# Optimization experiments

Hardware: AMD Instinct MI355X
Metric: run time of the kernel (lower is better)

The kernel has to match this reference:

```python
import jax, jax.numpy as jnp
import numpy as np

D_MODEL, Q, V, H = 1024, 64, 64, 16
B, K = 2, 2048


def setup_inputs() -> dict:
    key = jax.random.key(0)
    ks = jax.random.split(key, 8)
    s = 0.02
    return {
        "xi": jax.random.normal(ks[0], (B, K, D_MODEL), dtype=jnp.float32),
        # stacked per-head projection weights (equivalent to h separate nn.Linear)
        "Wq": jax.random.normal(ks[1], (H, D_MODEL, Q), dtype=jnp.float32) * s,
        "bq": jax.random.normal(ks[2], (H, Q), dtype=jnp.float32) * s,
        "Wk": jax.random.normal(ks[3], (H, D_MODEL, Q), dtype=jnp.float32) * s,
        "bk": jax.random.normal(ks[4], (H, Q), dtype=jnp.float32) * s,
        "Wv": jax.random.normal(ks[5], (H, D_MODEL, V), dtype=jnp.float32) * s,
        "bv": jax.random.normal(ks[6], (H, V), dtype=jnp.float32) * s,
        "Wo": jax.random.normal(ks[7], (H * V, D_MODEL), dtype=jnp.float32) * s,
        "bo": jnp.zeros((D_MODEL,), dtype=jnp.float32),
    }


def reference(xi, Wq, bq, Wk, bk, Wv, bv, Wo, bo):
    # per-head projections, batched over heads: [B,H,K,q]
    queries = jnp.einsum("bkd,hdq->bhkq", xi, Wq) + bq[None, :, None, :]
    keys = jnp.einsum("bkd,hdq->bhkq", xi, Wk) + bk[None, :, None, :]
    values = jnp.einsum("bkd,hdv->bhkv", xi, Wv) + bv[None, :, None, :]
    # NOTE: original scales by sqrt(queries.shape[1]) == sqrt(seq_len K), not sqrt(q)
    scale = 1.0 / np.sqrt(xi.shape[1]).astype(np.float32)
    scores = jax.nn.softmax(jnp.einsum("bhkq,bhmq->bhkm", queries, keys) * scale, axis=-1)
    attn = jnp.einsum("bhkm,bhmv->bhkv", scores, values)  # [B,H,K,v]
    # concat heads along last dim -> [B,K,H*v]
    attn = attn.transpose(0, 2, 1, 3).reshape(xi.shape[0], xi.shape[1], -1)
    return attn @ Wo + bo
```

## Files before the change

### kernel.cpp

```cpp
#include <hip/hip_runtime.h>
#include <math.h>

typedef __bf16 bf16x8 __attribute__((ext_vector_type(8)));
typedef float  f32x4  __attribute__((ext_vector_type(4)));
typedef float  f32x16 __attribute__((ext_vector_type(16)));
typedef unsigned short u16x8 __attribute__((ext_vector_type(8)));

#define D_MODEL 1024
#define QDIM    64
#define HEADS   16
#define BATCH   2
#define SEQ     2048
#define M_ROWS  (BATCH*SEQ)
#define NCAT    (HEADS*3*QDIM)

__device__ __forceinline__ unsigned short f2bf(float f) {
    unsigned int u = __float_as_uint(f);
    u += 0x7fffu + ((u >> 16) & 1u);
    return (unsigned short)(u >> 16);
}

__device__ __forceinline__ void gl16(const unsigned short* g, unsigned short* l) {
    __builtin_amdgcn_global_load_lds(
        (const __attribute__((address_space(1))) unsigned int*)g,
        (__attribute__((address_space(3))) unsigned int*)l, 16, 0, 0);
}

__global__ __launch_bounds__(256) void k_cvt_bf16(const float* __restrict__ in,
                                                  unsigned short* __restrict__ out) {
    int i = (blockIdx.x * 256 + threadIdx.x) * 8;
    f32x4 a = *(const f32x4*)(in + i);
    f32x4 b = *(const f32x4*)(in + i + 4);
    u16x8 o;
    o[0]=f2bf(a[0]); o[1]=f2bf(a[1]); o[2]=f2bf(a[2]); o[3]=f2bf(a[3]);
    o[4]=f2bf(b[0]); o[5]=f2bf(b[1]); o[6]=f2bf(b[2]); o[7]=f2bf(b[3]);
    *(u16x8*)(out + i) = o;
}

__global__ __launch_bounds__(256) void k_prep_w(const float* __restrict__ Wq,
                                                const float* __restrict__ Wk,
                                                const float* __restrict__ Wv,
                                                const float* __restrict__ bq,
                                                const float* __restrict__ bk,
                                                const float* __restrict__ bv,
                                                const float* __restrict__ Wo,
                                                unsigned short* __restrict__ WcatT,
                                                float* __restrict__ bcat,
                                                unsigned short* __restrict__ WoT,
                                                float qscale) {
    __shared__ float t[64][65];
    int tid = threadIdx.x;
    int dr = tid >> 2, qc = (tid & 3) * 16;
    if (blockIdx.x < 768) {
        int blk = blockIdx.x;
        int dt = blk & 15, h = (blk >> 4) & 15, s = blk >> 8;
        const float* W = (s == 0) ? Wq : (s == 1) ? Wk : Wv;
        float sc = (s == 0) ? qscale : 1.0f;
        const float* src = W + (size_t)h * (D_MODEL * QDIM) + (size_t)(dt * 64 + dr) * QDIM + qc;
#pragma unroll
        for (int j = 0; j < 4; ++j) {
            f32x4 v = *(const f32x4*)(src + j * 4);
            t[dr][qc + j * 4 + 0] = v[0]; t[dr][qc + j * 4 + 1] = v[1];
            t[dr][qc + j * 4 + 2] = v[2]; t[dr][qc + j * 4 + 3] = v[3];
        }
        __syncthreads();
        int q = tid >> 2, dc = (tid & 3) * 16;
        unsigned short* dst = WcatT + (size_t)(h * 192 + s * 64 + q) * D_MODEL + dt * 64 + dc;
#pragma unroll
        for (int j = 0; j < 2; ++j) {
            u16x8 o;
#pragma unroll
            for (int e = 0; e < 8; ++e) o[e] = f2bf(t[dc + j * 8 + e][q] * sc);
            *(u16x8*)(dst + j * 8) = o;
        }
        if (dt == 0 && tid < 64) {
            const float* bb = (s == 0) ? bq : (s == 1) ? bk : bv;
            bcat[h * 192 + s * 64 + tid] = bb[h * QDIM + tid] * sc;
        }
    } else {
        int blk = blockIdx.x - 768;
        int ct = blk & 15, rt = blk >> 4;
        const float* src = Wo + (size_t)(rt * 64 + dr) * D_MODEL + ct * 64 + qc;
#pragma unroll
        for (int j = 0; j < 4; ++j) {
            f32x4 v = *(const f32x4*)(src + j * 4);
            t[dr][qc + j * 4 + 0] = v[0]; t[dr][qc + j * 4 + 1] = v[1];
            t[dr][qc + j * 4 + 2] = v[2]; t[dr][qc + j * 4 + 3] = v[3];
        }
        __syncthreads();
        int q = tid >> 2, dc = (tid & 3) * 16;
        unsigned short* dst = WoT + (size_t)(ct * 64 + q) * D_MODEL + rt * 64 + dc;
#pragma unroll
        for (int j = 0; j < 2; ++j) {
            u16x8 o;
#pragma unroll
            for (int e = 0; e < 8; ++e) o[e] = f2bf(t[dc + j * 8 + e][q]);
            *(u16x8*)(dst + j * 8) = o;
        }
    }
}

template<bool OUT_BF16>
__global__ __launch_bounds__(256) void k_gemm(const unsigned short* __restrict__ A,
                                              const unsigned short* __restrict__ BT,
                                              const float* __restrict__ bias,
                                              void* __restrict__ Cout,
                                              int N, int Kd) {
    __shared__ __align__(16) unsigned char smem[65536];
    const int tid = threadIdx.x;
    const int lane = tid & 63, w = tid >> 6;
    const int g = lane >> 4, c = lane & 15;
    int nwg = gridDim.x * gridDim.y;
    int bid = blockIdx.y * gridDim.x + blockIdx.x;
    int sw = (bid & 7) * (nwg >> 3) + (bid >> 3);
    int bx = sw % gridDim.x, by = sw / gridDim.x;
    const int m0 = by * 128, n0 = bx * 128;
    const int wm = (w >> 1) * 64, wn = (w & 1) * 64;
    f32x4 acc[4][4] = {};

    const int srow = w * 16 + (lane >> 2);
    const int scol = ((lane & 3) ^ ((lane >> 3) & 3)) * 8;
    const unsigned short* pA0 = A  + (size_t)(m0 + srow) * Kd + scol;
    const unsigned short* pA1 = pA0 + (size_t)64 * Kd;
    const unsigned short* pB0 = BT + (size_t)(n0 + srow) * Kd + scol;
    const unsigned short* pB1 = pB0 + (size_t)64 * Kd;
    const int kc = (c >> 1) & 3;
    const int aoff = (wm + c) * 64 + ((g ^ kc) * 16);
    const int boff = (wn + c) * 64 + ((g ^ kc) * 16);

#define STAGE(buf)                                                                   \
    {                                                                                \
        unsigned short* lb = (unsigned short*)(smem + (buf) * 16384) + w * 512;      \
        gl16(pA0, lb);                                                               \
        gl16(pA1, lb + 2048);                                                        \
        gl16(pB0, lb + 4096);                                                        \
        gl16(pB1, lb + 6144);                                                        \
        pA0 += 32; pA1 += 32; pB0 += 32; pB1 += 32;                                  \
    }

#define COMPUTE(buf)                                                                 \
    {                                                                                \
        const unsigned char* Ab = smem + (buf) * 16384;                              \
        const unsigned char* Bb = Ab + 8192;                                         \
        bf16x8 af[4], bfr[4];                                                        \
        _Pragma("unroll") for (int mf = 0; mf < 4; ++mf)                             \
            af[mf] = *(const bf16x8*)(Ab + mf * 1024 + aoff);                        \
        _Pragma("unroll") for (int nf = 0; nf < 4; ++nf)                             \
            bfr[nf] = *(const bf16x8*)(Bb + nf * 1024 + boff);                       \
        __builtin_amdgcn_s_setprio(1);                                               \
        _Pragma("unroll") for (int mf = 0; mf < 4; ++mf)                             \
            _Pragma("unroll") for (int nf = 0; nf < 4; ++nf)                         \
                acc[mf][nf] = __builtin_amdgcn_mfma_f32_16x16x32_bf16(               \
                    af[mf], bfr[nf], acc[mf][nf], 0, 0, 0);                          \
        __builtin_amdgcn_s_setprio(0);                                               \
    }

    const int nt = Kd >> 5;
    STAGE(0); STAGE(1); STAGE(2);

    for (int t = 0; t < nt - 3; ++t) {
        STAGE((t + 3) & 3);
        asm volatile("s_waitcnt vmcnt(12)" ::: "memory");
        __builtin_amdgcn_s_barrier();
        __builtin_amdgcn_sched_barrier(0);
        COMPUTE(t & 3);
        __builtin_amdgcn_sched_barrier(0);
        __builtin_amdgcn_s_barrier();
    }
    asm volatile("s_waitcnt vmcnt(8)" ::: "memory");
    __builtin_amdgcn_s_barrier();
    __builtin_amdgcn_sched_barrier(0);
    COMPUTE((nt - 3) & 3);
    __builtin_amdgcn_sched_barrier(0);
    __builtin_amdgcn_s_barrier();
    asm volatile("s_waitcnt vmcnt(4)" ::: "memory");
    __builtin_amdgcn_s_barrier();
    __builtin_amdgcn_sched_barrier(0);
    COMPUTE((nt - 2) & 3);
    __builtin_amdgcn_sched_barrier(0);
    __builtin_amdgcn_s_barrier();
    asm volatile("s_waitcnt vmcnt(0)" ::: "memory");
    __builtin_amdgcn_s_barrier();
    __builtin_amdgcn_sched_barrier(0);
    COMPUTE((nt - 1) & 3);
#undef STAGE
#undef COMPUTE

#pragma unroll
    for (int mf = 0; mf < 4; ++mf)
#pragma unroll
        for (int nf = 0; nf < 4; ++nf) {
            int col = n0 + wn + nf * 16 + c;
            float bb = bias[col];
#pragma unroll
            for (int r = 0; r < 4; ++r) {
                int row = m0 + wm + mf * 16 + 4 * g + r;
                float v = acc[mf][nf][r] + bb;
                if (OUT_BF16)
                    ((unsigned short*)Cout)[(size_t)row * N + col] = f2bf(v);
                else
                    ((float*)Cout)[(size_t)row * N + col] = v;
            }
        }
}

__global__ __launch_bounds__(256) void k_repack(const unsigned short* __restrict__ qkv,
                                                unsigned short* __restrict__ kfrag,
                                                unsigned short* __restrict__ vfrag) {
    int blk = blockIdx.x;
    int kt = blk & 31, h = (blk >> 5) & 15, b = blk >> 9;
    __shared__ unsigned short ktile[64][72];
    __shared__ unsigned short vtile[64][72];
    int tid = threadIdx.x;
#pragma unroll
    for (int j = 0; j < 2; ++j) {
        int cid = tid + j * 256;
        int row = cid >> 3, ch = (cid & 7) * 8;
        const unsigned short* base = qkv + (size_t)(b * SEQ + kt * 64 + row) * NCAT + h * 192;
        *(u16x8*)&ktile[row][ch] = *(const u16x8*)(base + 64 + ch);
        *(u16x8*)&vtile[row][ch] = *(const u16x8*)(base + 128 + ch);
    }
    __syncthreads();
    size_t obase = (size_t)blk * 4096;
#pragma unroll
    for (int j = 0; j < 2; ++j) {
        int p = tid + j * 256;
        int f = p >> 6, l31 = p & 31, hi = (p >> 5) & 1;
        *(u16x8*)(kfrag + obase + p * 8) =
            *(const u16x8*)&ktile[(f >> 2) * 32 + l31][(f & 3) * 16 + hi * 8];
        int vv = (f & 1) * 32 + l31;
        int k0 = (f >> 2) * 32 + ((f >> 1) & 1) * 16 + hi * 8;
        u16x8 o;
#pragma unroll
        for (int e = 0; e < 8; ++e) o[e] = vtile[k0 + e][vv];
        *(u16x8*)(vfrag + obase + p * 8) = o;
    }
}

__global__ __launch_bounds__(256) void k_attn(const unsigned short* __restrict__ qkv,
                                              const unsigned short* __restrict__ kfrag,
                                              const unsigned short* __restrict__ vfrag,
                                              unsigned short* __restrict__ attn) {
    int bid = blockIdx.x;
    int blk = (bid & 7) * 128 + (bid >> 3);
    int qt = blk & 31, h = (blk >> 5) & 15, b = blk >> 9;
    int tid = threadIdx.x, w = tid >> 6, lane = tid & 63;
    int l31 = lane & 31, hi = lane >> 5;
    int qh = w & 1, kh = w >> 1;

    __shared__ float red[4096];
    __shared__ float rsb[128];

    const int qbase = b * SEQ + qt * 64;
    const unsigned short* qrow = qkv + (size_t)(qbase + qh * 32 + l31) * NCAT + h * 192;
    bf16x8 qf0 = *(const bf16x8*)(qrow + 0 * 16 + hi * 8);
    bf16x8 qf1 = *(const bf16x8*)(qrow + 1 * 16 + hi * 8);
    bf16x8 qf2 = *(const bf16x8*)(qrow + 2 * 16 + hi * 8);
    bf16x8 qf3 = *(const bf16x8*)(qrow + 3 * 16 + hi * 8);

    f32x16 o0 = {}, o1 = {};
    float rsum = 0.f;

    const size_t fb = (size_t)(b * 512 + h * 32) * 4096 + (size_t)(kh * 4) * 512 + lane * 8;
    const unsigned short* kp = kfrag + fb;
    const unsigned short* vp = vfrag + fb;

    bf16x8 aK0, aK1, aK2, aK3, aV0, aV1, aV2, aV3;
    bf16x8 bK0, bK1, bK2, bK3, bV0, bV1, bV2, bV3;

#define LOADT(K0, K1, K2, K3, V0, V1, V2, V3)                   \
    {                                                           \
        K0 = *(const bf16x8*)(kp);                              \
        K1 = *(const bf16x8*)(kp + 512);                        \
        K2 = *(const bf16x8*)(kp + 1024);                       \
        K3 = *(const bf16x8*)(kp + 1536);                       \
        V0 = *(const bf16x8*)(vp);                              \
        V1 = *(const bf16x8*)(vp + 512);                        \
        V2 = *(const bf16x8*)(vp + 1024);                       \
        V3 = *(const bf16x8*)(vp + 1536);                       \
        kp += 4096; vp += 4096;                                 \
    }

#define COMPUTE(K0, K1, K2, K3, V0, V1, V2, V3)                                       \
    {                                                                                 \
        f32x16 st = {};                                                               \
        st = __builtin_amdgcn_mfma_f32_32x32x16_bf16(K0, qf0, st, 0, 0, 0);           \
        st = __builtin_amdgcn_mfma_f32_32x32x16_bf16(K1, qf1, st, 0, 0, 0);           \
        st = __builtin_amdgcn_mfma_f32_32x32x16_bf16(K2, qf2, st, 0, 0, 0);           \
        st = __builtin_amdgcn_mfma_f32_32x32x16_bf16(K3, qf3, st, 0, 0, 0);           \
        _Pragma("unroll") for (int r = 0; r < 16; ++r) {                              \
            float p = __builtin_amdgcn_exp2f(st[r]);                                  \
            st[r] = p;                                                                \
            rsum += p;                                                                \
        }                                                                             \
        unsigned int d0, d1, d2, d3, d4, d5, d6, d7;                                  \
        asm("v_cvt_pk_bf16_f32 %0, %1, %2" : "=v"(d0) : "v"(st[0]),  "v"(st[1]));     \
        asm("v_cvt_pk_bf16_f32 %0, %1, %2" : "=v"(d1) : "v"(st[2]),  "v"(st[3]));     \
        asm("v_cvt_pk_bf16_f32 %0, %1, %2" : "=v"(d2) : "v"(st[4]),  "v"(st[5]));     \
        asm("v_cvt_pk_bf16_f32 %0, %1, %2" : "=v"(d3) : "v"(st[6]),  "v"(st[7]));     \
        asm("v_cvt_pk_bf16_f32 %0, %1, %2" : "=v"(d4) : "v"(st[8]),  "v"(st[9]));     \
        asm("v_cvt_pk_bf16_f32 %0, %1, %2" : "=v"(d5) : "v"(st[10]), "v"(st[11]));    \
        asm("v_cvt_pk_bf16_f32 %0, %1, %2" : "=v"(d6) : "v"(st[12]), "v"(st[13]));    \
        asm("v_cvt_pk_bf16_f32 %0, %1, %2" : "=v"(d7) : "v"(st[14]), "v"(st[15]));    \
        asm("v_permlane32_swap_b32 %0, %1" : "+v"(d0), "+v"(d2));                     \
        asm("v_permlane32_swap_b32 %0, %1" : "+v"(d1), "+v"(d3));                     \
        asm("v_permlane32_swap_b32 %0, %1" : "+v"(d4), "+v"(d6));                     \
        asm("v_permlane32_swap_b32 %0, %1" : "+v"(d5), "+v"(d7));                     \
        union { unsigned int u[4]; bf16x8 v; } pa0, pa1;                              \
        pa0.u[0] = d0; pa0.u[1] = d1; pa0.u[2] = d2; pa0.u[3] = d3;                   \
        pa1.u[0] = d4; pa1.u[1] = d5; pa1.u[2] = d6; pa1.u[3] = d7;                   \
        o0 = __builtin_amdgcn_mfma_f32_32x32x16_bf16(pa0.v, V0, o0, 0, 0, 0);         \
        o1 = __builtin_amdgcn_mfma_f32_32x32x16_bf16(pa0.v, V1, o1, 0, 0, 0);         \
        o0 = __builtin_amdgcn_mfma_f32_32x32x16_bf16(pa1.v, V2, o0, 0, 0, 0);         \
        o1 = __builtin_amdgcn_mfma_f32_32x32x16_bf16(pa1.v, V3, o1, 0, 0, 0);         \
    }

    LOADT(aK0, aK1, aK2, aK3, aV0, aV1, aV2, aV3);

    const int NT = SEQ / 64;
    for (int t = 0; t < NT; t += 2) {
        LOADT(bK0, bK1, bK2, bK3, bV0, bV1, bV2, bV3);
        COMPUTE(aK0, aK1, aK2, aK3, aV0, aV1, aV2, aV3);
        if (t + 2 < NT)
            LOADT(aK0, aK1, aK2, aK3, aV0, aV1, aV2, aV3);
        COMPUTE(bK0, bK1, bK2, bK3, bV0, bV1, bV2, bV3);
    }
#undef LOADT
#undef COMPUTE

    rsum += __shfl_xor(rsum, 32);
    if (kh == 1) {
#pragma unroll
        for (int r = 0; r < 16; ++r) {
            int q = (r & 3) + 8 * (r >> 2) + 4 * hi;
            red[(qh * 32 + q) * 64 + l31]      = o0[r];
            red[(qh * 32 + q) * 64 + 32 + l31] = o1[r];
        }
    }
    if (lane < 32) rsb[(kh * 2 + qh) * 32 + l31] = rsum;
    __syncthreads();
    if (kh == 0) {
#pragma unroll
        for (int r = 0; r < 16; ++r) {
            int q = (r & 3) + 8 * (r >> 2) + 4 * hi;
            float tot = rsb[qh * 32 + q] + rsb[(2 + qh) * 32 + q];
            float inv = 1.0f / tot;
            float v0 = (o0[r] + red[(qh * 32 + q) * 64 + l31]) * inv;
            float v1 = (o1[r] + red[(qh * 32 + q) * 64 + 32 + l31]) * inv;
            int row = qbase + qh * 32 + q;
            attn[(size_t)row * (HEADS * QDIM) + h * QDIM + l31]      = f2bf(v0);
            attn[(size_t)row * (HEADS * QDIM) + h * QDIM + 32 + l31] = f2bf(v1);
        }
    }
}

extern "C" void kernel_launch(void* const* d_in, const int* in_sizes, int n_in,
                              void* d_out, int out_size, void* d_ws, size_t ws_size,
                              hipStream_t stream) {
    const float* xi = (const float*)d_in[0];
    const float* Wq = (const float*)d_in[1];
    const float* bq = (const float*)d_in[2];
    const float* Wk = (const float*)d_in[3];
    const float* bk = (const float*)d_in[4];
    const float* Wv = (const float*)d_in[5];
    const float* bv = (const float*)d_in[6];
    const float* Wo = (const float*)d_in[7];
    const float* bo = (const float*)d_in[8];

    unsigned short* xi_bf = (unsigned short*)d_ws;
    unsigned short* WcatT = xi_bf + (size_t)M_ROWS * D_MODEL;
    unsigned short* WoT   = WcatT + (size_t)NCAT * D_MODEL;
    float*          bcat  = (float*)(WoT + (size_t)D_MODEL * D_MODEL);
    unsigned short* qkvc  = (unsigned short*)(bcat + NCAT);
    unsigned short* kfrag = qkvc + (size_t)M_ROWS * NCAT;
    unsigned short* vfrag = kfrag + (size_t)BATCH * HEADS * 32 * 4096;
    unsigned short* attnb = vfrag + (size_t)BATCH * HEADS * 32 * 4096;

    float qscale = 1.4426950408889634f / sqrtf((float)SEQ);

    k_cvt_bf16<<<(M_ROWS * D_MODEL) / 2048, 256, 0, stream>>>(xi, xi_bf);
    k_prep_w<<<1024, 256, 0, stream>>>(Wq, Wk, Wv, bq, bk, bv, Wo, WcatT, bcat, WoT, qscale);

    k_gemm<true><<<dim3(NCAT / 128, M_ROWS / 128), 256, 0, stream>>>(
        xi_bf, WcatT, bcat, (void*)qkvc, NCAT, D_MODEL);

    k_repack<<<BATCH * HEADS * (SEQ / 64), 256, 0, stream>>>(qkvc, kfrag, vfrag);

    k_attn<<<BATCH * HEADS * (SEQ / 64), 256, 0, stream>>>(qkvc, kfrag, vfrag, attnb);

    k_gemm<false><<<dim3(D_MODEL / 128, M_ROWS / 128), 256, 0, stream>>>(
        attnb, WoT, bo, d_out, D_MODEL, D_MODEL);
}
```

Baseline: 119.6 us.

## Software-pipeline attention loop so QK^T MFMA of next tile overlaps exp/PV

Splits the per-tile attention body into separate QK^T, exp/pack and PV stages and interleaves them across two key tiles. The QK^T MFMAs of the second tile are issued before the PV MFMAs of the first, so matrix-core work overlaps the exp and conversion VALU work. V fragments now use one shared register set loaded just before use instead of double-buffered, which lowers register pressure but exposes V load latency more. Adds a second score accumulator, which raises live registers.

```diff
diff --git a/kernel.cpp b/kernel.cpp
--- a/kernel.cpp
+++ b/kernel.cpp
@@ -265,68 +265,87 @@
     const unsigned short* kp = kfrag + fb;
     const unsigned short* vp = vfrag + fb;
 
-    bf16x8 aK0, aK1, aK2, aK3, aV0, aV1, aV2, aV3;
-    bf16x8 bK0, bK1, bK2, bK3, bV0, bV1, bV2, bV3;
-
-#define LOADT(K0, K1, K2, K3, V0, V1, V2, V3)                   \
+    bf16x8 aK0, aK1, aK2, aK3, bK0, bK1, bK2, bK3;
+    bf16x8 v0, v1, v2, v3;
+    f32x16 sa, sb;
+    union PU { unsigned int u[4]; bf16x8 v; } paa0, paa1, pab0, pab1;
+
+#define LOADK(K0, K1, K2, K3)                                   \
     {                                                           \
         K0 = *(const bf16x8*)(kp);                              \
         K1 = *(const bf16x8*)(kp + 512);                        \
         K2 = *(const bf16x8*)(kp + 1024);                       \
         K3 = *(const bf16x8*)(kp + 1536);                       \
-        V0 = *(const bf16x8*)(vp);                              \
-        V1 = *(const bf16x8*)(vp + 512);                        \
-        V2 = *(const bf16x8*)(vp + 1024);                       \
-        V3 = *(const bf16x8*)(vp + 1536);                       \
-        kp += 4096; vp += 4096;                                 \
-    }
-
-#define COMPUTE(K0, K1, K2, K3, V0, V1, V2, V3)                                       \
+        kp += 4096;                                             \
+    }
+#define LOADV()                                                 \
+    {                                                           \
+        v0 = *(const bf16x8*)(vp);                              \
+        v1 = *(const bf16x8*)(vp + 512);                        \
+        v2 = *(const bf16x8*)(vp + 1024);                       \
+        v3 = *(const bf16x8*)(vp + 1536);                       \
+        vp += 4096;                                             \
+    }
+#define QKT(S, K0, K1, K2, K3)                                              \
+    {                                                                       \
+        S = (f32x16){};                                                     \
+        S = __builtin_amdgcn_mfma_f32_32x32x16_bf16(K0, qf0, S, 0, 0, 0);   \
+        S = __builtin_amdgcn_mfma_f32_32x32x16_bf16(K1, qf1, S, 0, 0, 0);   \
+        S = __builtin_amdgcn_mfma_f32_32x32x16_bf16(K2, qf2, S, 0, 0, 0);   \
+        S = __builtin_amdgcn_mfma_f32_32x32x16_bf16(K3, qf3, S, 0, 0, 0);   \
+    }
+#define EXPPACK(S, PA0, PA1)                                                          \
     {                                                                                 \
-        f32x16 st = {};                                                               \
-        st = __builtin_amdgcn_mfma_f32_32x32x16_bf16(K0, qf0, st, 0, 0, 0);           \
-        st = __builtin_amdgcn_mfma_f32_32x32x16_bf16(K1, qf1, st, 0, 0, 0);           \
-        st = __builtin_amdgcn_mfma_f32_32x32x16_bf16(K2, qf2, st, 0, 0, 0);           \
-        st = __builtin_amdgcn_mfma_f32_32x32x16_bf16(K3, qf3, st, 0, 0, 0);           \
         _Pragma("unroll") for (int r = 0; r < 16; ++r) {                              \
-            float p = __builtin_amdgcn_exp2f(st[r]);                                  \
-            st[r] = p;                                                                \
+            float p = __builtin_amdgcn_exp2f(S[r]);                                   \
+            S[r] = p;                                                                 \
             rsum += p;                                                                \
         }                                                                             \
         unsigned int d0, d1, d2, d3, d4, d5, d6, d7;                                  \
-        asm("v_cvt_pk_bf16_f32 %0, %1, %2" : "=v"(d0) : "v"(st[0]),  "v"(st[1]));     \
-        asm("v_cvt_pk_bf16_f32 %0, %1, %2" : "=v"(d1) : "v"(st[2]),  "v"(st[3]));     \
-        asm("v_cvt_pk_bf16_f32 %0, %1, %2" : "=v"(d2) : "v"(st[4]),  "v"(st[5]));     \
-        asm("v_cvt_pk_bf16_f32 %0, %1, %2" : "=v"(d3) : "v"(st[6]),  "v"(st[7]));     \
-        asm("v_cvt_pk_bf16_f32 %0, %1, %2" : "=v"(d4) : "v"(st[8]),  "v"(st[9]));     \
-        asm("v_cvt_pk_bf16_f32 %0, %1, %2" : "=v"(d5) : "v"(st[10]), "v"(st[11]));    \
-        asm("v_cvt_pk_bf16_f32 %0, %1, %2" : "=v"(d6) : "v"(st[12]), "v"(st[13]));    \
-        asm("v_cvt_pk_bf16_f32 %0, %1, %2" : "=v"(d7) : "v"(st[14]), "v"(st[15]));    \
+        asm("v_cvt_pk_bf16_f32 %0, %1, %2" : "=v"(d0) : "v"(S[0]),  "v"(S[1]));       \
+        asm("v_cvt_pk_bf16_f32 %0, %1, %2" : "=v"(d1) : "v"(S[2]),  "v"(S[3]));       \
+        asm("v_cvt_pk_bf16_f32 %0, %1, %2" : "=v"(d2) : "v"(S[4]),  "v"(S[5]));       \
+        asm("v_cvt_pk_bf16_f32 %0, %1, %2" : "=v"(d3) : "v"(S[6]),  "v"(S[7]));       \
+        asm("v_cvt_pk_bf16_f32 %0, %1, %2" : "=v"(d4) : "v"(S[8]),  "v"(S[9]));       \
+        asm("v_cvt_pk_bf16_f32 %0, %1, %2" : "=v"(d5) : "v"(S[10]), "v"(S[11]));      \
+        asm("v_cvt_pk_bf16_f32 %0, %1, %2" : "=v"(d6) : "v"(S[12]), "v"(S[13]));      \
+        asm("v_cvt_pk_bf16_f32 %0, %1, %2" : "=v"(d7) : "v"(S[14]), "v"(S[15]));      \
         asm("v_permlane32_swap_b32 %0, %1" : "+v"(d0), "+v"(d2));                     \
         asm("v_permlane32_swap_b32 %0, %1" : "+v"(d1), "+v"(d3));                     \
         asm("v_permlane32_swap_b32 %0, %1" : "+v"(d4), "+v"(d6));                     \
         asm("v_permlane32_swap_b32 %0, %1" : "+v"(d5), "+v"(d7));                     \
-        union { unsigned int u[4]; bf16x8 v; } pa0, pa1;                              \
-        pa0.u[0] = d0; pa0.u[1] = d1; pa0.u[2] = d2; pa0.u[3] = d3;                   \
-        pa1.u[0] = d4; pa1.u[1] = d5; pa1.u[2] = d6; pa1.u[3] = d7;                   \
-        o0 = __builtin_amdgcn_mfma_f32_32x32x16_bf16(pa0.v, V0, o0, 0, 0, 0);         \
-        o1 = __builtin_amdgcn_mfma_f32_32x32x16_bf16(pa0.v, V1, o1, 0, 0, 0);         \
-        o0 = __builtin_amdgcn_mfma_f32_32x32x16_bf16(pa1.v, V2, o0, 0, 0, 0);         \
-        o1 = __builtin_amdgcn_mfma_f32_32x32x16_bf16(pa1.v, V3, o1, 0, 0, 0);         \
-    }
-
-    LOADT(aK0, aK1, aK2, aK3, aV0, aV1, aV2, aV3);
+        PA0.u[0] = d0; PA0.u[1] = d1; PA0.u[2] = d2; PA0.u[3] = d3;                   \
+        PA1.u[0] = d4; PA1.u[1] = d5; PA1.u[2] = d6; PA1.u[3] = d7;                   \
+    }
+#define PV(PA0, PA1)                                                                  \
+    {                                                                                 \
+        o0 = __builtin_amdgcn_mfma_f32_32x32x16_bf16(PA0.v, v0, o0, 0, 0, 0);         \
+        o1 = __builtin_amdgcn_mfma_f32_32x32x16_bf16(PA0.v, v1, o1, 0, 0, 0);         \
+        o0 = __builtin_amdgcn_mfma_f32_32x32x16_bf16(PA1.v, v2, o0, 0, 0, 0);         \
+        o1 = __builtin_amdgcn_mfma_f32_32x32x16_bf16(PA1.v, v3, o1, 0, 0, 0);         \
+    }
+
+    LOADK(aK0, aK1, aK2, aK3);
 
     const int NT = SEQ / 64;
     for (int t = 0; t < NT; t += 2) {
-        LOADT(bK0, bK1, bK2, bK3, bV0, bV1, bV2, bV3);
-        COMPUTE(aK0, aK1, aK2, aK3, aV0, aV1, aV2, aV3);
+        LOADV();
+        LOADK(bK0, bK1, bK2, bK3);
+        QKT(sa, aK0, aK1, aK2, aK3);
+        EXPPACK(sa, paa0, paa1);
         if (t + 2 < NT)
-            LOADT(aK0, aK1, aK2, aK3, aV0, aV1, aV2, aV3);
-        COMPUTE(bK0, bK1, bK2, bK3, bV0, bV1, bV2, bV3);
-    }
-#undef LOADT
-#undef COMPUTE
+            LOADK(aK0, aK1, aK2, aK3);
+        QKT(sb, bK0, bK1, bK2, bK3);
+        PV(paa0, paa1);
+        LOADV();
+        EXPPACK(sb, pab0, pab1);
+        PV(pab0, pab1);
+    }
+#undef LOADK
+#undef LOADV
+#undef QKT
+#undef EXPPACK
+#undef PV
 
     rsum += __shfl_xor(rsum, 32);
     if (kh == 1) {
@@ -345,11 +364,11 @@
             int q = (r & 3) + 8 * (r >> 2) + 4 * hi;
             float tot = rsb[qh * 32 + q] + rsb[(2 + qh) * 32 + q];
             float inv = 1.0f / tot;
-            float v0 = (o0[r] + red[(qh * 32 + q) * 64 + l31]) * inv;
-            float v1 = (o1[r] + red[(qh * 32 + q) * 64 + 32 + l31]) * inv;
+            float v0e = (o0[r] + red[(qh * 32 + q) * 64 + l31]) * inv;
+            float v1e = (o1[r] + red[(qh * 32 + q) * 64 + 32 + l31]) * inv;
             int row = qbase + qh * 32 + q;
-            attn[(size_t)row * (HEADS * QDIM) + h * QDIM + l31]      = f2bf(v0);
-            attn[(size_t)row * (HEADS * QDIM) + h * QDIM + 32 + l31] = f2bf(v1);
+            attn[(size_t)row * (HEADS * QDIM) + h * QDIM + l31]      = f2bf(v0e);
+            attn[(size_t)row * (HEADS * QDIM) + h * QDIM + 32 + l31] = f2bf(v1e);
         }
     }
 }
```

Result: no change. 120.2 us (+0.6%).

## Merge input conversion into weight prep and restructure GEMM to double-buffered BK=64

Applied to the files above, without the earlier changes.

Folds the xi fp32-to-bf16 conversion into the weight-prep kernel as extra blocks, which removes one kernel launch. The GEMM K-loop changes from a 4-stage, BK=32 pipeline to a 2-stage, BK=64 double buffer with an XOR-swizzled LDS layout and two MFMA sub-steps per tile. LDS use stays at 64KB. The shallower pipeline may hide less global-load latency, though each barrier now covers more compute.

```diff
diff --git a/kernel.cpp b/kernel.cpp
--- a/kernel.cpp
+++ b/kernel.cpp
@@ -26,33 +26,34 @@
         (__attribute__((address_space(3))) unsigned int*)l, 16, 0, 0);
 }
 
-__global__ __launch_bounds__(256) void k_cvt_bf16(const float* __restrict__ in,
-                                                  unsigned short* __restrict__ out) {
-    int i = (blockIdx.x * 256 + threadIdx.x) * 8;
-    f32x4 a = *(const f32x4*)(in + i);
-    f32x4 b = *(const f32x4*)(in + i + 4);
-    u16x8 o;
-    o[0]=f2bf(a[0]); o[1]=f2bf(a[1]); o[2]=f2bf(a[2]); o[3]=f2bf(a[3]);
-    o[4]=f2bf(b[0]); o[5]=f2bf(b[1]); o[6]=f2bf(b[2]); o[7]=f2bf(b[3]);
-    *(u16x8*)(out + i) = o;
-}
-
-__global__ __launch_bounds__(256) void k_prep_w(const float* __restrict__ Wq,
+__global__ __launch_bounds__(256) void k_prep_w(const float* __restrict__ xi,
+                                                const float* __restrict__ Wq,
                                                 const float* __restrict__ Wk,
                                                 const float* __restrict__ Wv,
                                                 const float* __restrict__ bq,
                                                 const float* __restrict__ bk,
                                                 const float* __restrict__ bv,
                                                 const float* __restrict__ Wo,
+                                                unsigned short* __restrict__ xi_bf,
                                                 unsigned short* __restrict__ WcatT,
                                                 float* __restrict__ bcat,
                                                 unsigned short* __restrict__ WoT,
                                                 float qscale) {
+    int tid = threadIdx.x;
+    if (blockIdx.x < 2048) {
+        int i = (blockIdx.x * 256 + tid) * 8;
+        f32x4 a = *(const f32x4*)(xi + i);
+        f32x4 b = *(const f32x4*)(xi + i + 4);
+        u16x8 o;
+        o[0]=f2bf(a[0]); o[1]=f2bf(a[1]); o[2]=f2bf(a[2]); o[3]=f2bf(a[3]);
+        o[4]=f2bf(b[0]); o[5]=f2bf(b[1]); o[6]=f2bf(b[2]); o[7]=f2bf(b[3]);
+        *(u16x8*)(xi_bf + i) = o;
+        return;
+    }
     __shared__ float t[64][65];
-    int tid = threadIdx.x;
     int dr = tid >> 2, qc = (tid & 3) * 16;
-    if (blockIdx.x < 768) {
-        int blk = blockIdx.x;
+    if (blockIdx.x < 2816) {
+        int blk = blockIdx.x - 2048;
         int dt = blk & 15, h = (blk >> 4) & 15, s = blk >> 8;
         const float* W = (s == 0) ? Wq : (s == 1) ? Wk : Wv;
         float sc = (s == 0) ? qscale : 1.0f;
@@ -78,7 +79,7 @@
             bcat[h * 192 + s * 64 + tid] = bb[h * QDIM + tid] * sc;
         }
     } else {
-        int blk = blockIdx.x - 768;
+        int blk = blockIdx.x - 2816;
         int ct = blk & 15, rt = blk >> 4;
         const float* src = Wo + (size_t)(rt * 64 + dr) * D_MODEL + ct * 64 + qc;
 #pragma unroll
@@ -106,7 +107,8 @@
                                               const float* __restrict__ bias,
                                               void* __restrict__ Cout,
                                               int N, int Kd) {
-    __shared__ __align__(16) unsigned char smem[65536];
+    __shared__ __align__(16) unsigned short Alds[2][128 * 64];
+    __shared__ __align__(16) unsigned short Blds[2][128 * 64];
     const int tid = threadIdx.x;
     const int lane = tid & 63, w = tid >> 6;
     const int g = lane >> 4, c = lane & 15;
@@ -116,73 +118,58 @@
     int bx = sw % gridDim.x, by = sw / gridDim.x;
     const int m0 = by * 128, n0 = bx * 128;
     const int wm = (w >> 1) * 64, wn = (w & 1) * 64;
+    const int r8 = lane >> 3, chx = (lane & 7) ^ r8;
+    const int swz = c & 7;
     f32x4 acc[4][4] = {};
 
-    const int srow = w * 16 + (lane >> 2);
-    const int scol = ((lane & 3) ^ ((lane >> 3) & 3)) * 8;
-    const unsigned short* pA0 = A  + (size_t)(m0 + srow) * Kd + scol;
-    const unsigned short* pA1 = pA0 + (size_t)64 * Kd;
-    const unsigned short* pB0 = BT + (size_t)(n0 + srow) * Kd + scol;
-    const unsigned short* pB1 = pB0 + (size_t)64 * Kd;
-    const int kc = (c >> 1) & 3;
-    const int aoff = (wm + c) * 64 + ((g ^ kc) * 16);
-    const int boff = (wn + c) * 64 + ((g ^ kc) * 16);
-
-#define STAGE(buf)                                                                   \
-    {                                                                                \
-        unsigned short* lb = (unsigned short*)(smem + (buf) * 16384) + w * 512;      \
-        gl16(pA0, lb);                                                               \
-        gl16(pA1, lb + 2048);                                                        \
-        gl16(pB0, lb + 4096);                                                        \
-        gl16(pB1, lb + 6144);                                                        \
-        pA0 += 32; pA1 += 32; pB0 += 32; pB1 += 32;                                  \
-    }
-
-#define COMPUTE(buf)                                                                 \
-    {                                                                                \
-        const unsigned char* Ab = smem + (buf) * 16384;                              \
-        const unsigned char* Bb = Ab + 8192;                                         \
-        bf16x8 af[4], bfr[4];                                                        \
-        _Pragma("unroll") for (int mf = 0; mf < 4; ++mf)                             \
-            af[mf] = *(const bf16x8*)(Ab + mf * 1024 + aoff);                        \
-        _Pragma("unroll") for (int nf = 0; nf < 4; ++nf)                             \
-            bfr[nf] = *(const bf16x8*)(Bb + nf * 1024 + boff);                       \
-        __builtin_amdgcn_s_setprio(1);                                               \
-        _Pragma("unroll") for (int mf = 0; mf < 4; ++mf)                             \
-            _Pragma("unroll") for (int nf = 0; nf < 4; ++nf)                         \
-                acc[mf][nf] = __builtin_amdgcn_mfma_f32_16x16x32_bf16(               \
-                    af[mf], bfr[nf], acc[mf][nf], 0, 0, 0);                          \
-        __builtin_amdgcn_s_setprio(0);                                               \
-    }
-
-    const int nt = Kd >> 5;
-    STAGE(0); STAGE(1); STAGE(2);
-
-    for (int t = 0; t < nt - 3; ++t) {
-        STAGE((t + 3) & 3);
-        asm volatile("s_waitcnt vmcnt(12)" ::: "memory");
+    const unsigned short* pA = A  + (size_t)m0 * Kd;
+    const unsigned short* pB = BT + (size_t)n0 * Kd;
+    int k0 = 0;
+
+#define STAGE(buf)                                                                       \
+    {                                                                                    \
+        _Pragma("unroll") for (int i = 0; i < 4; ++i) {                                  \
+            int row = w * 32 + i * 8 + r8;                                               \
+            gl16(pA + (size_t)row * Kd + k0 + chx * 8, &Alds[buf][w * 2048 + i * 512]);  \
+            gl16(pB + (size_t)row * Kd + k0 + chx * 8, &Blds[buf][w * 2048 + i * 512]);  \
+        }                                                                                \
+        k0 += 64;                                                                        \
+    }
+
+#define COMPUTE(buf)                                                                     \
+    {                                                                                    \
+        _Pragma("unroll") for (int kk = 0; kk < 2; ++kk) {                               \
+            bf16x8 af[4], bfr[4];                                                        \
+            _Pragma("unroll") for (int mf = 0; mf < 4; ++mf)                             \
+                af[mf] = *(const bf16x8*)(&Alds[buf][(wm + mf * 16 + c) * 64 +           \
+                                                     (((kk * 4 + g) ^ swz) * 8)]);      \
+            _Pragma("unroll") for (int nf = 0; nf < 4; ++nf)                             \
+                bfr[nf] = *(const bf16x8*)(&Blds[buf][(wn + nf * 16 + c) * 64 +          \
+                                                      (((kk * 4 + g) ^ swz) * 8)]);     \
+            __builtin_amdgcn_s_setprio(1);                                               \
+            _Pragma("unroll") for (int mf = 0; mf < 4; ++mf)                             \
+                _Pragma("unroll") for (int nf = 0; nf < 4; ++nf)                         \
+                    acc[mf][nf] = __builtin_amdgcn_mfma_f32_16x16x32_bf16(               \
+                        af[mf], bfr[nf], acc[mf][nf], 0, 0, 0);                          \
+            __builtin_amdgcn_s_setprio(0);                                               \
+        }                                                                                \
+    }
+
+    const int nt = Kd >> 6;
+    STAGE(0);
+    for (int t = 0; t < nt; ++t) {
+        if (t + 1 < nt) {
+            STAGE((t + 1) & 1);
+            asm volatile("s_waitcnt vmcnt(8)" ::: "memory");
+        } else {
+            asm volatile("s_waitcnt vmcnt(0)" ::: "memory");
+        }
         __builtin_amdgcn_s_barrier();
         __builtin_amdgcn_sched_barrier(0);
-        COMPUTE(t & 3);
+        COMPUTE(t & 1);
         __builtin_amdgcn_sched_barrier(0);
         __builtin_amdgcn_s_barrier();
     }
-    asm volatile("s_waitcnt vmcnt(8)" ::: "memory");
-    __builtin_amdgcn_s_barrier();
-    __builtin_amdgcn_sched_barrier(0);
-    COMPUTE((nt - 3) & 3);
-    __builtin_amdgcn_sched_barrier(0);
-    __builtin_amdgcn_s_barrier();
-    asm volatile("s_waitcnt vmcnt(4)" ::: "memory");
-    __builtin_amdgcn_s_barrier();
-    __builtin_amdgcn_sched_barrier(0);
-    COMPUTE((nt - 2) & 3);
-    __builtin_amdgcn_sched_barrier(0);
-    __builtin_amdgcn_s_barrier();
-    asm volatile("s_waitcnt vmcnt(0)" ::: "memory");
-    __builtin_amdgcn_s_barrier();
-    __builtin_amdgcn_sched_barrier(0);
-    COMPUTE((nt - 1) & 3);
 #undef STAGE
 #undef COMPUTE
 
@@ -345,11 +332,11 @@
             int q = (r & 3) + 8 * (r >> 2) + 4 * hi;
             float tot = rsb[qh * 32 + q] + rsb[(2 + qh) * 32 + q];
             float inv = 1.0f / tot;
-            float v0 = (o0[r] + red[(qh * 32 + q) * 64 + l31]) * inv;
-            float v1 = (o1[r] + red[(qh * 32 + q) * 64 + 32 + l31]) * inv;
+            float v0e = (o0[r] + red[(qh * 32 + q) * 64 + l31]) * inv;
+            float v1e = (o1[r] + red[(qh * 32 + q) * 64 + 32 + l31]) * inv;
             int row = qbase + qh * 32 + q;
-            attn[(size_t)row * (HEADS * QDIM) + h * QDIM + l31]      = f2bf(v0);
-            attn[(size_t)row * (HEADS * QDIM) + h * QDIM + 32 + l31] = f2bf(v1);
+            attn[(size_t)row * (HEADS * QDIM) + h * QDIM + l31]      = f2bf(v0e);
+            attn[(size_t)row * (HEADS * QDIM) + h * QDIM + 32 + l31] = f2bf(v1e);
         }
     }
 }
@@ -378,8 +365,8 @@
 
     float qscale = 1.4426950408889634f / sqrtf((float)SEQ);
 
-    k_cvt_bf16<<<(M_ROWS * D_MODEL) / 2048, 256, 0, stream>>>(xi, xi_bf);
-    k_prep_w<<<1024, 256, 0, stream>>>(Wq, Wk, Wv, bq, bk, bv, Wo, WcatT, bcat, WoT, qscale);
+    k_prep_w<<<3072, 256, 0, stream>>>(xi, Wq, Wk, Wv, bq, bk, bv, Wo,
+                                       xi_bf, WcatT, bcat, WoT, qscale);
 
     k_gemm<true><<<dim3(NCAT / 128, M_ROWS / 128), 256, 0, stream>>>(
         xi_bf, WcatT, bcat, (void*)qkvc, NCAT, D_MODEL);
```

New measurement: 127.8 us. 1.07x slower.

## Fuse K/V fragment repack into QKV projection GEMM epilogue

Applied to the files above, without the earlier changes.

The QKV GEMM epilogue now writes K and V values straight into the MFMA fragment layouts used by the attention kernel, and only Q goes to the concatenated qkv buffer. This removes the separate repack kernel launch and its read-back of K/V from global memory. In exchange, the epilogue does scattered 2-byte and 8-byte stores with per-element index arithmetic, which may coalesce worse than the previous row-major writes.

```diff
diff --git a/kernel.cpp b/kernel.cpp
--- a/kernel.cpp
+++ b/kernel.cpp
@@ -5,6 +5,7 @@
 typedef float  f32x4  __attribute__((ext_vector_type(4)));
 typedef float  f32x16 __attribute__((ext_vector_type(16)));
 typedef unsigned short u16x8 __attribute__((ext_vector_type(8)));
+typedef unsigned short u16x4 __attribute__((ext_vector_type(4)));
 
 #define D_MODEL 1024
 #define QDIM    64
@@ -100,11 +101,13 @@
     }
 }
 
-template<bool OUT_BF16>
+template<bool FUSED>
 __global__ __launch_bounds__(256) void k_gemm(const unsigned short* __restrict__ A,
                                               const unsigned short* __restrict__ BT,
                                               const float* __restrict__ bias,
                                               void* __restrict__ Cout,
+                                              unsigned short* __restrict__ kfrag,
+                                              unsigned short* __restrict__ vfrag,
                                               int N, int Kd) {
     __shared__ __align__(16) unsigned char smem[65536];
     const int tid = threadIdx.x;
@@ -187,53 +190,50 @@
 #undef COMPUTE
 
 #pragma unroll
-    for (int mf = 0; mf < 4; ++mf)
+    for (int mf = 0; mf < 4; ++mf) {
+        const int row0 = m0 + wm + mf * 16 + 4 * g;
+        const int bb_  = row0 >> 11;
+        const int s_   = row0 & 2047;
+        const int tile = s_ >> 6;
+        const int krb  = s_ & 63;
 #pragma unroll
         for (int nf = 0; nf < 4; ++nf) {
             int col = n0 + wn + nf * 16 + c;
-            float bb = bias[col];
-#pragma unroll
-            for (int r = 0; r < 4; ++r) {
-                int row = m0 + wm + mf * 16 + 4 * g + r;
-                float v = acc[mf][nf][r] + bb;
-                if (OUT_BF16)
-                    ((unsigned short*)Cout)[(size_t)row * N + col] = f2bf(v);
-                else
-                    ((float*)Cout)[(size_t)row * N + col] = v;
+            float bv = bias[col];
+            if (!FUSED) {
+#pragma unroll
+                for (int r = 0; r < 4; ++r)
+                    ((float*)Cout)[(size_t)(row0 + r) * N + col] = acc[mf][nf][r] + bv;
+            } else {
+                unsigned short q0 = f2bf(acc[mf][nf][0] + bv);
+                unsigned short q1 = f2bf(acc[mf][nf][1] + bv);
+                unsigned short q2 = f2bf(acc[mf][nf][2] + bv);
+                unsigned short q3 = f2bf(acc[mf][nf][3] + bv);
+                int h   = col / 192;
+                int rem = col - h * 192;
+                int kind = rem >> 6;
+                int d   = rem & 63;
+                if (kind == 0) {
+                    unsigned short* p = (unsigned short*)Cout + (size_t)row0 * NCAT + col;
+                    p[0] = q0; p[NCAT] = q1; p[2 * NCAT] = q2; p[3 * NCAT] = q3;
+                } else {
+                    size_t obase = (size_t)(bb_ * 512 + h * 32 + tile) * 4096;
+                    if (kind == 1) {
+                        int f  = (krb >> 5) * 4 + (d >> 4);
+                        int hi = (d >> 3) & 1;
+                        unsigned short* p = kfrag + obase + f * 512 + hi * 256 +
+                                            (size_t)(krb & 31) * 8 + (d & 7);
+                        p[0] = q0; p[8] = q1; p[16] = q2; p[24] = q3;
+                    } else {
+                        int f  = (krb >> 5) * 4 + ((krb >> 4) & 1) * 2 + (d >> 5);
+                        int hi = (krb >> 3) & 1;
+                        u16x4 pk = {q0, q1, q2, q3};
+                        *(u16x4*)(vfrag + obase + f * 512 + hi * 256 +
+                                  (size_t)(d & 31) * 8 + (krb & 7)) = pk;
+                    }
+                }
             }
         }
-}
-
-__global__ __launch_bounds__(256) void k_repack(const unsigned short* __restrict__ qkv,
-                                                unsigned short* __restrict__ kfrag,
-                                                unsigned short* __restrict__ vfrag) {
-    int blk = blockIdx.x;
-    int kt = blk & 31, h = (blk >> 5) & 15, b = blk >> 9;
-    __shared__ unsigned short ktile[64][72];
-    __shared__ unsigned short vtile[64][72];
-    int tid = threadIdx.x;
-#pragma unroll
-    for (int j = 0; j < 2; ++j) {
-        int cid = tid + j * 256;
-        int row = cid >> 3, ch = (cid & 7) * 8;
-        const unsigned short* base = qkv + (size_t)(b * SEQ + kt * 64 + row) * NCAT + h * 192;
-        *(u16x8*)&ktile[row][ch] = *(const u16x8*)(base + 64 + ch);
-        *(u16x8*)&vtile[row][ch] = *(const u16x8*)(base + 128 + ch);
-    }
-    __syncthreads();
-    size_t obase = (size_t)blk * 4096;
-#pragma unroll
-    for (int j = 0; j < 2; ++j) {
-        int p = tid + j * 256;
-        int f = p >> 6, l31 = p & 31, hi = (p >> 5) & 1;
-        *(u16x8*)(kfrag + obase + p * 8) =
-            *(const u16x8*)&ktile[(f >> 2) * 32 + l31][(f & 3) * 16 + hi * 8];
-        int vv = (f & 1) * 32 + l31;
-        int k0 = (f >> 2) * 32 + ((f >> 1) & 1) * 16 + hi * 8;
-        u16x8 o;
-#pragma unroll
-        for (int e = 0; e < 8; ++e) o[e] = vtile[k0 + e][vv];
-        *(u16x8*)(vfrag + obase + p * 8) = o;
     }
 }
 
@@ -345,11 +345,11 @@
             int q = (r & 3) + 8 * (r >> 2) + 4 * hi;
             float tot = rsb[qh * 32 + q] + rsb[(2 + qh) * 32 + q];
             float inv = 1.0f / tot;
-            float v0 = (o0[r] + red[(qh * 32 + q) * 64 + l31]) * inv;
-            float v1 = (o1[r] + red[(qh * 32 + q) * 64 + 32 + l31]) * inv;
+            float v0e = (o0[r] + red[(qh * 32 + q) * 64 + l31]) * inv;
+            float v1e = (o1[r] + red[(qh * 32 + q) * 64 + 32 + l31]) * inv;
             int row = qbase + qh * 32 + q;
-            attn[(size_t)row * (HEADS * QDIM) + h * QDIM + l31]      = f2bf(v0);
-            attn[(size_t)row * (HEADS * QDIM) + h * QDIM + 32 + l31] = f2bf(v1);
+            attn[(size_t)row * (HEADS * QDIM) + h * QDIM + l31]      = f2bf(v0e);
+            attn[(size_t)row * (HEADS * QDIM) + h * QDIM + 32 + l31] = f2bf(v1e);
         }
     }
 }
@@ -382,12 +382,10 @@
     k_prep_w<<<1024, 256, 0, stream>>>(Wq, Wk, Wv, bq, bk, bv, Wo, WcatT, bcat, WoT, qscale);
 
     k_gemm<true><<<dim3(NCAT / 128, M_ROWS / 128), 256, 0, stream>>>(
-        xi_bf, WcatT, bcat, (void*)qkvc, NCAT, D_MODEL);
-
-    k_repack<<<BATCH * HEADS * (SEQ / 64), 256, 0, stream>>>(qkvc, kfrag, vfrag);
+        xi_bf, WcatT, bcat, (void*)qkvc, kfrag, vfrag, NCAT, D_MODEL);
 
     k_attn<<<BATCH * HEADS * (SEQ / 64), 256, 0, stream>>>(qkvc, kfrag, vfrag, attnb);
 
     k_gemm<false><<<dim3(D_MODEL / 128, M_ROWS / 128), 256, 0, stream>>>(
-        attnb, WoT, bo, d_out, D_MODEL, D_MODEL);
-}
+        attnb, WoT, bo, d_out, nullptr, nullptr, D_MODEL, D_MODEL);
+}
```

Result: faster. 116.9 us (-2.2%).
